# Kernel optimization log

Measured on AMD Instinct MI355X. Metric: run time of the kernel, lower is better.

## Reference

```python
import jax, jax.numpy as jnp
import numpy as np

DIM = 768
HEADS = 12
HEAD_DIM = DIM // HEADS
ROPE_BASE = 100.0  # Dust3R uses freq=100 for its rotary embedding


def apply_rope(x):
    # x: [B, H, N, D] -> rotary embedding over token index (rotate-half form)
    B, H, N, D = x.shape
    pos = jnp.arange(N, dtype=jnp.float32)
    inv_freq = 1.0 / (ROPE_BASE ** (jnp.arange(0, D, 2, dtype=jnp.float32) / D))
    ang = pos[:, None] * inv_freq[None, :]            # [N, D/2]
    cos = jnp.concatenate([jnp.cos(ang), jnp.cos(ang)], axis=-1).astype(x.dtype)  # [N, D]
    sin = jnp.concatenate([jnp.sin(ang), jnp.sin(ang)], axis=-1).astype(x.dtype)
    x1, x2 = jnp.split(x, 2, axis=-1)
    x_rot = jnp.concatenate([-x2, x1], axis=-1)
    return x * cos + x_rot * sin


def setup_inputs() -> dict:
    key = jax.random.key(0)
    ks = jax.random.split(key, 8)
    B, N = 8, 1024
    scale = 0.02
    return {
        "query": jax.random.normal(ks[0], (B, N, DIM), jnp.float32),
        "key": jax.random.normal(ks[1], (B, N, DIM), jnp.float32),
        "value": jax.random.normal(ks[2], (B, N, DIM), jnp.float32),
        "Wq": jax.random.normal(ks[3], (DIM, DIM), jnp.float32) * scale,
        "Wk": jax.random.normal(ks[4], (DIM, DIM), jnp.float32) * scale,
        "Wv": jax.random.normal(ks[5], (DIM, DIM), jnp.float32) * scale,
        "Wo": jax.random.normal(ks[6], (DIM, DIM), jnp.float32) * scale,
        "bo": jax.random.normal(ks[7], (DIM,), jnp.float32) * scale,
    }


def reference(query, key, value, Wq, Wk, Wv, Wo, bo):
    B, Nq, C = query.shape
    H, D = HEADS, HEAD_DIM
    sm_scale = D ** -0.5
    # Linear projections (torch Linear: x @ W.T), split heads -> [B, H, N, D]
    q = jnp.einsum('bnc,dc->bnd', query, Wq).reshape(B, Nq, H, D).transpose(0, 2, 1, 3)
    k = jnp.einsum('bnc,dc->bnd', key, Wk).reshape(B, -1, H, D).transpose(0, 2, 1, 3)
    v = jnp.einsum('bnc,dc->bnd', value, Wv).reshape(B, -1, H, D).transpose(0, 2, 1, 3)
    q = apply_rope(q)
    k = apply_rope(k)
    attn = jnp.einsum('bhqd,bhkd->bhqk', q, k) * sm_scale
    attn = jax.nn.softmax(attn, axis=-1)
    x = jnp.einsum('bhqk,bhkd->bhqd', attn, v)
    x = x.transpose(0, 2, 1, 3).reshape(B, Nq, C)
    return jnp.einsum('bnc,dc->bnd', x, Wo) + bo
```

## Files before the change

### kernel.cpp

```cpp
#include <hip/hip_runtime.h>
#include <cmath>

typedef __bf16 bf16x8 __attribute__((ext_vector_type(8)));
typedef float f32x4 __attribute__((ext_vector_type(4)));
typedef unsigned short u16;

#define MFMA_BF16 __builtin_amdgcn_mfma_f32_16x16x32_bf16

__device__ __forceinline__ u16 f2bf(float f) {
  unsigned int u = __float_as_uint(f);
  u = (u + 0x7fffu + ((u >> 16) & 1u)) >> 16;
  return (u16)u;
}

__device__ __forceinline__ unsigned pbf(float f) {
  return (__float_as_uint(f) + 0x8000u) >> 16;
}

__device__ __forceinline__ void async16(const u16* g, u16* l) {
  __builtin_amdgcn_global_load_lds(
      (__attribute__((address_space(1))) void*)g,
      (__attribute__((address_space(3))) void*)l, 16, 0, 0);
}

__global__ __launch_bounds__(256) void cvt_bf16(const float4* __restrict__ in,
                                                uint2* __restrict__ out, int n4) {
  int i = blockIdx.x * 256 + threadIdx.x;
  if (i >= n4) return;
  float4 f = in[i];
  uint2 o;
  o.x = (unsigned)f2bf(f.x) | ((unsigned)f2bf(f.y) << 16);
  o.y = (unsigned)f2bf(f.z) | ((unsigned)f2bf(f.w) << 16);
  out[i] = o;
}

__global__ __launch_bounds__(256) void cvt_all(
    const float4* s0, const float4* s1, const float4* s2, const float4* s3,
    const float4* s4, const float4* s5, const float4* s6,
    uint2* d0, uint2* d1, uint2* d2, uint2* d3, uint2* d4, uint2* d5, uint2* d6) {
  int i = blockIdx.x * 256 + threadIdx.x;
  const float4* src;
  uint2* dst;
  int off;
  if (i < 1572864)      { src = s0; dst = d0; off = i; }
  else if (i < 3145728) { src = s1; dst = d1; off = i - 1572864; }
  else if (i < 4718592) { src = s2; dst = d2; off = i - 3145728; }
  else {
    int j = i - 4718592;
    int w = j / 147456;
    off = j - w * 147456;
    src = (w == 0) ? s3 : (w == 1) ? s4 : (w == 2) ? s5 : s6;
    dst = (w == 0) ? d3 : (w == 1) ? d4 : (w == 2) ? d5 : d6;
  }
  float4 f = src[off];
  uint2 o;
  o.x = (unsigned)f2bf(f.x) | ((unsigned)f2bf(f.y) << 16);
  o.y = (unsigned)f2bf(f.z) | ((unsigned)f2bf(f.w) << 16);
  dst[off] = o;
}

__device__ __forceinline__ void gemm_body(const u16* __restrict__ Ag,
                                          const u16* __restrict__ Wg,
                                          void* __restrict__ OutP,
                                          const float* __restrict__ bias,
                                          int mode, int bx, int by) {
  __shared__ alignas(16) u16 As[2][128][64];
  __shared__ alignas(16) u16 Bs[2][64][64];
  const int tid  = threadIdx.x;
  const int lane = tid & 63, wv = tid >> 6;
  const int l15  = lane & 15, quad = lane >> 4;
  const int row0 = bx * 128, col0 = by * 64;
  const int wm = wv * 32;
  const int swA = l15 & 7;

  size_t aSrc[4], bSrc[2];
  int aDst[4], bDst[2];
#pragma unroll
  for (int rr = 0; rr < 4; ++rr) {
    int c = rr * 256 + tid;
    int row = c >> 3, cp = c & 7;
    int gc = cp ^ (row & 7);
    aSrc[rr] = (size_t)(row0 + row) * 768 + gc * 8;
    aDst[rr] = c * 8;
  }
#pragma unroll
  for (int rr = 0; rr < 2; ++rr) {
    int c = rr * 256 + tid;
    int row = c >> 3, cp = c & 7;
    int gc = cp ^ (row & 7);
    bSrc[rr] = (size_t)(col0 + row) * 768 + gc * 8;
    bDst[rr] = c * 8;
  }

  auto stage = [&](int kb, int bf) {
#pragma unroll
    for (int rr = 0; rr < 4; ++rr) async16(&Ag[aSrc[rr] + kb], &((u16*)As[bf])[aDst[rr]]);
#pragma unroll
    for (int rr = 0; rr < 2; ++rr) async16(&Wg[bSrc[rr] + kb], &((u16*)Bs[bf])[bDst[rr]]);
  };

  f32x4 acc[2][4];
#pragma unroll
  for (int i = 0; i < 2; ++i)
#pragma unroll
    for (int j = 0; j < 4; ++j) acc[i][j] = (f32x4){0.f, 0.f, 0.f, 0.f};

  stage(0, 0);
  __syncthreads();

  auto step = [&](int kb, int rb) {
    if (kb < 704) stage(kb + 64, rb ^ 1);
#pragma unroll
    for (int kd = 0; kd < 2; ++kd) {
      int cpk = (((kd * 4 + quad) ^ swA)) * 8;
      bf16x8 af[2], bfr[4];
      af[0] = *(const bf16x8*)&As[rb][wm + l15][cpk];
      af[1] = *(const bf16x8*)&As[rb][wm + 16 + l15][cpk];
#pragma unroll
      for (int nt = 0; nt < 4; ++nt) bfr[nt] = *(const bf16x8*)&Bs[rb][nt * 16 + l15][cpk];
#pragma unroll
      for (int mt = 0; mt < 2; ++mt)
#pragma unroll
        for (int nt = 0; nt < 4; ++nt)
          acc[mt][nt] = MFMA_BF16(af[mt], bfr[nt], acc[mt][nt], 0, 0, 0);
    }
    __syncthreads();
  };

  for (int kb = 0; kb < 768; kb += 128) {
    step(kb, 0);
    step(kb + 64, 1);
  }

  if (mode == 3) {
    float* O = (float*)OutP;
#pragma unroll
    for (int mt = 0; mt < 2; ++mt)
#pragma unroll
      for (int r = 0; r < 4; ++r) {
        int m = row0 + wm + mt * 16 + quad * 4 + r;
#pragma unroll
        for (int nt = 0; nt < 4; ++nt) {
          int c = col0 + nt * 16 + l15;
          O[(size_t)m * 768 + c] = acc[mt][nt][r] + bias[c];
        }
      }
  } else if (mode == 2) {
    u16* O = (u16*)OutP;
#pragma unroll
    for (int mt = 0; mt < 2; ++mt)
#pragma unroll
      for (int r = 0; r < 4; ++r) {
        int m = row0 + wm + mt * 16 + quad * 4 + r;
        int b = m >> 10, n = m & 1023;
#pragma unroll
        for (int nt = 0; nt < 4; ++nt) {
          int c = col0 + nt * 16 + l15;
          O[(size_t)(b * 768 + c) * 1024 + n] = f2bf(acc[mt][nt][r]);
        }
      }
  } else {
    u16* O = (u16*)OutP;
    const float scale = (mode == 0) ? 0.125f * 1.44269504088896f : 1.0f;
    const float invf0 = exp2f(-6.6438561897747395f * (float)l15 * (1.0f / 32.0f));
    const float invf1 = exp2f(-6.6438561897747395f * (float)(16 + l15) * (1.0f / 32.0f));
#pragma unroll
    for (int mt = 0; mt < 2; ++mt)
#pragma unroll
      for (int r = 0; r < 4; ++r) {
        int m = row0 + wm + mt * 16 + quad * 4 + r;
        int b = m >> 10, n = m & 1023;
        float fn = (float)n;
        size_t rowbase = (size_t)b * 786432 + (size_t)n * 64;
#pragma unroll
        for (int nt = 0; nt < 2; ++nt) {
          float sv, cv;
          __sincosf(fn * (nt ? invf1 : invf0), &sv, &cv);
          float x1 = acc[mt][nt][r], x2 = acc[mt][nt + 2][r];
          int c1 = col0 + nt * 16 + l15;
          int c2 = c1 + 32;
          O[rowbase + (size_t)(c1 >> 6) * 65536 + (c1 & 63)] = f2bf((x1 * cv - x2 * sv) * scale);
          O[rowbase + (size_t)(c2 >> 6) * 65536 + (c2 & 63)] = f2bf((x2 * cv + x1 * sv) * scale);
        }
      }
  }
}

__global__ __launch_bounds__(256, 3) void gemm768(const u16* __restrict__ A,
                                                  const u16* __restrict__ W,
                                                  void* __restrict__ OutP,
                                                  const float* __restrict__ bias,
                                                  int mode) {
  gemm_body(A, W, OutP, bias, mode, blockIdx.x, blockIdx.y);
}

__global__ __launch_bounds__(256, 3) void gemm_qkv(
    const u16* __restrict__ xq, const u16* __restrict__ xk, const u16* __restrict__ xv,
    const u16* __restrict__ wq, const u16* __restrict__ wk, const u16* __restrict__ wv,
    u16* __restrict__ qb, u16* __restrict__ kb, u16* __restrict__ vtb) {
  int z = blockIdx.z;
  const u16* A = (z == 0) ? xq : (z == 1) ? xk : xv;
  const u16* W = (z == 0) ? wq : (z == 1) ? wk : wv;
  void* O      = (z == 0) ? (void*)qb : (z == 1) ? (void*)kb : (void*)vtb;
  gemm_body(A, W, O, nullptr, z, blockIdx.x, blockIdx.y);
}

__global__ __launch_bounds__(256, 3) void attn_fused(const u16* __restrict__ Q,
                                                     const u16* __restrict__ K,
                                                     const u16* __restrict__ Vt,
                                                     u16* __restrict__ X) {
  __shared__ alignas(16) u16 KsF[2][4096];
  __shared__ alignas(16) u16 VsF[2][4096];
  __shared__ alignas(16) u16 Ps[4][2304];

  const int tid  = threadIdx.x;
  const int lane = tid & 63, wv = tid >> 6;
  const int l15  = lane & 15, quad = lane >> 4;
  const int bh = blockIdx.x, qt = blockIdx.y;
  const size_t base = (size_t)bh * 65536;
  const int sw8 = (quad ^ ((l15 >> 1) & 3)) * 8;

  const u16* Qg = Q + base + (size_t)qt * 8192;
  const u16* Kb = K + base;
  const u16* Vb = Vt + base;

  int kOff[2], vOff[2], dOff[2];
#pragma unroll
  for (int rr = 0; rr < 2; ++rr) {
    int c = rr * 256 + tid;
    int sub = c >> 8, rowi = (c >> 2) & 63, colc = c & 3;
    int cs = (colc ^ ((rowi >> 1) & 3)) * 8;
    kOff[rr] = rowi * 64 + sub * 32 + cs;
    vOff[rr] = rowi * 1024 + sub * 32 + cs;
    dOff[rr] = c * 8;
  }

  auto stageKV = [&](int kt, int bf) {
#pragma unroll
    for (int rr = 0; rr < 2; ++rr) {
      async16(&Kb[(size_t)kt * 64 + kOff[rr]], &KsF[bf][dOff[rr]]);
      async16(&Vb[(size_t)kt + vOff[rr]], &VsF[bf][dOff[rr]]);
    }
  };

  u16* Pflat = &Ps[0][0];
#pragma unroll
  for (int rr = 0; rr < 4; ++rr) {
    int c = rr * 256 + tid;
    async16(&Qg[c * 8], &Pflat[c * 8]);
  }
  stageKV(0, 0);
  __syncthreads();

  bf16x8 qf[2][2];
#pragma unroll
  for (int mt = 0; mt < 2; ++mt)
#pragma unroll
    for (int kd = 0; kd < 2; ++kd)
      qf[mt][kd] = *(const bf16x8*)&Pflat[(wv * 32 + mt * 16 + l15) * 64 + kd * 32 + quad * 8];
  __syncthreads();

  f32x4 o[2][4];
  float lsum[2] = {0.f, 0.f};
#pragma unroll
  for (int mt = 0; mt < 2; ++mt)
#pragma unroll
    for (int nt = 0; nt < 4; ++nt) o[mt][nt] = (f32x4){0.f, 0.f, 0.f, 0.f};

  u16* Pw = &Ps[wv][0];
  const int prow0 = l15 * 72, prow1 = (16 + l15) * 72;

  auto tile = [&](int t, int rb) {
    if (t < 15) stageKV((t + 1) * 64, rb ^ 1);

    f32x4 s[2][4];
#pragma unroll
    for (int ct = 0; ct < 4; ++ct) {
      bf16x8 kf0 = *(const bf16x8*)&KsF[rb][(ct * 16 + l15) * 32 + sw8];
      bf16x8 kf1 = *(const bf16x8*)&KsF[rb][2048 + (ct * 16 + l15) * 32 + sw8];
#pragma unroll
      for (int mt = 0; mt < 2; ++mt) {
        f32x4 tacc = (f32x4){0.f, 0.f, 0.f, 0.f};
        tacc = MFMA_BF16(kf0, qf[mt][0], tacc, 0, 0, 0);
        tacc = MFMA_BF16(kf1, qf[mt][1], tacc, 0, 0, 0);
        s[mt][ct] = tacc;
      }
    }

#pragma unroll
    for (int mt = 0; mt < 2; ++mt) {
#pragma unroll
      for (int ct = 0; ct < 4; ++ct) {
        float p0 = __builtin_amdgcn_exp2f(s[mt][ct][0]);
        float p1 = __builtin_amdgcn_exp2f(s[mt][ct][1]);
        float p2 = __builtin_amdgcn_exp2f(s[mt][ct][2]);
        float p3 = __builtin_amdgcn_exp2f(s[mt][ct][3]);
        lsum[mt] += (p0 + p1) + (p2 + p3);
        uint2 w;
        w.x = pbf(p0) | (pbf(p1) << 16);
        w.y = pbf(p2) | (pbf(p3) << 16);
        *(uint2*)&Pw[(mt ? prow1 : prow0) + ct * 16 + quad * 4] = w;
      }
    }

#pragma unroll
    for (int ks = 0; ks < 2; ++ks) {
      bf16x8 pf0 = *(const bf16x8*)&Pw[prow0 + ks * 32 + quad * 8];
      bf16x8 pf1 = *(const bf16x8*)&Pw[prow1 + ks * 32 + quad * 8];
#pragma unroll
      for (int nt = 0; nt < 4; ++nt) {
        bf16x8 vf = *(const bf16x8*)&VsF[rb][ks * 2048 + (nt * 16 + l15) * 32 + sw8];
        o[0][nt] = MFMA_BF16(vf, pf0, o[0][nt], 0, 0, 0);
        o[1][nt] = MFMA_BF16(vf, pf1, o[1][nt], 0, 0, 0);
      }
    }
    __syncthreads();
  };

  for (int t = 0; t < 16; t += 2) {
    tile(t, 0);
    tile(t + 1, 1);
  }

  const int b = bh / 12, h = bh % 12;
#pragma unroll
  for (int mt = 0; mt < 2; ++mt) {
    float l = lsum[mt];
    l += __shfl_xor(l, 16);
    l += __shfl_xor(l, 32);
    float inv = __builtin_amdgcn_rcpf(l);
    int n = qt * 128 + wv * 32 + mt * 16 + l15;
    size_t rowoff = ((size_t)(b * 1024 + n)) * 768 + h * 64 + quad * 4;
#pragma unroll
    for (int nt = 0; nt < 4; ++nt) {
      uint2 w;
      w.x = (unsigned)f2bf(o[mt][nt][0] * inv) | ((unsigned)f2bf(o[mt][nt][1] * inv) << 16);
      w.y = (unsigned)f2bf(o[mt][nt][2] * inv) | ((unsigned)f2bf(o[mt][nt][3] * inv) << 16);
      *(uint2*)&X[rowoff + nt * 16] = w;
    }
  }
}

extern "C" void kernel_launch(void* const* d_in, const int* in_sizes, int n_in,
                              void* d_out, int out_size, void* d_ws, size_t ws_size,
                              hipStream_t stream) {
  const float* qin = (const float*)d_in[0];
  const float* kin = (const float*)d_in[1];
  const float* vin = (const float*)d_in[2];
  const float* Wq  = (const float*)d_in[3];
  const float* Wk  = (const float*)d_in[4];
  const float* Wv  = (const float*)d_in[5];
  const float* Wo  = (const float*)d_in[6];
  const float* bo  = (const float*)d_in[7];
  char* ws = (char*)d_ws;

  if (ws_size >= 80216064) {
    u16* xq16 = (u16*)(ws + 0);
    u16* xk16 = (u16*)(ws + 12582912);
    u16* xv16 = (u16*)(ws + 25165824);
    u16* qb   = (u16*)(ws + 37748736);
    u16* kb   = (u16*)(ws + 50331648);
    u16* vtb  = (u16*)(ws + 62914560);
    u16* wq16 = (u16*)(ws + 75497472);
    u16* wk16 = wq16 + 589824;
    u16* wv16 = wk16 + 589824;
    u16* wo16 = wv16 + 589824;
    u16* X    = xq16;

    cvt_all<<<20736, 256, 0, stream>>>(
        (const float4*)qin, (const float4*)kin, (const float4*)vin,
        (const float4*)Wq, (const float4*)Wk, (const float4*)Wv, (const float4*)Wo,
        (uint2*)xq16, (uint2*)xk16, (uint2*)xv16,
        (uint2*)wq16, (uint2*)wk16, (uint2*)wv16, (uint2*)wo16);
    gemm_qkv<<<dim3(64, 12, 3), 256, 0, stream>>>(xq16, xk16, xv16, wq16, wk16, wv16,
                                                  qb, kb, vtb);
    attn_fused<<<dim3(96, 8), 256, 0, stream>>>(qb, kb, vtb, X);
    gemm768<<<dim3(64, 12), 256, 0, stream>>>(X, wo16, d_out, bo, 3);
  } else {
    u16* xbuf = (u16*)(ws + 0);
    u16* qb   = (u16*)(ws + 12582912);
    u16* kb   = (u16*)(ws + 25165824);
    u16* vtb  = (u16*)(ws + 37748736);
    u16* wq16 = (u16*)(ws + 50331648);
    u16* wk16 = wq16 + 589824;
    u16* wv16 = wk16 + 589824;
    u16* wo16 = wv16 + 589824;

    cvt_bf16<<<576, 256, 0, stream>>>((const float4*)Wq, (uint2*)wq16, 147456);
    cvt_bf16<<<576, 256, 0, stream>>>((const float4*)Wk, (uint2*)wk16, 147456);
    cvt_bf16<<<576, 256, 0, stream>>>((const float4*)Wv, (uint2*)wv16, 147456);
    cvt_bf16<<<576, 256, 0, stream>>>((const float4*)Wo, (uint2*)wo16, 147456);

    dim3 ggrid(64, 12);
    cvt_bf16<<<6144, 256, 0, stream>>>((const float4*)qin, (uint2*)xbuf, 1572864);
    gemm768<<<ggrid, 256, 0, stream>>>(xbuf, wq16, (void*)qb, nullptr, 0);
    cvt_bf16<<<6144, 256, 0, stream>>>((const float4*)kin, (uint2*)xbuf, 1572864);
    gemm768<<<ggrid, 256, 0, stream>>>(xbuf, wk16, (void*)kb, nullptr, 1);
    cvt_bf16<<<6144, 256, 0, stream>>>((const float4*)vin, (uint2*)xbuf, 1572864);
    gemm768<<<ggrid, 256, 0, stream>>>(xbuf, wv16, (void*)vtb, nullptr, 2);

    attn_fused<<<dim3(96, 8), 256, 0, stream>>>(qb, kb, vtb, xbuf);

    gemm768<<<ggrid, 256, 0, stream>>>(xbuf, wo16, d_out, bo, 3);
  }
}
```

Before: 219.2 us.

## Enlarge GEMM tile to 128x128 with 2x2 warp layout, drop double buffering

The projection GEMM tile grows from 128x64 to 128x128, and each wave now computes a 64x64 sub-tile in a 2x2 arrangement instead of a 32x64 strip. This raises MFMA work per LDS fragment load and halves the grid's column count. The LDS double buffer is replaced by a single buffer with a load, sync, compute, sync loop, so global loads no longer overlap compute. Higher register use per thread (16 accumulators) may lower occupancy under the launch bound of 3.

```diff
diff --git a/kernel.cpp b/kernel.cpp
--- a/kernel.cpp
+++ b/kernel.cpp
@@ -64,98 +64,81 @@
                                           void* __restrict__ OutP,
                                           const float* __restrict__ bias,
                                           int mode, int bx, int by) {
-  __shared__ alignas(16) u16 As[2][128][64];
-  __shared__ alignas(16) u16 Bs[2][64][64];
+  __shared__ alignas(16) u16 As[128][64];
+  __shared__ alignas(16) u16 Bs[128][64];
   const int tid  = threadIdx.x;
   const int lane = tid & 63, wv = tid >> 6;
   const int l15  = lane & 15, quad = lane >> 4;
-  const int row0 = bx * 128, col0 = by * 64;
-  const int wm = wv * 32;
+  const int row0 = bx * 128, col0 = by * 128;
+  const int wr = (wv >> 1) * 64, wc = (wv & 1) * 64;
   const int swA = l15 & 7;
 
-  size_t aSrc[4], bSrc[2];
-  int aDst[4], bDst[2];
+  size_t aSrc[4], bSrc[4];
+  int dsts[4];
 #pragma unroll
   for (int rr = 0; rr < 4; ++rr) {
     int c = rr * 256 + tid;
     int row = c >> 3, cp = c & 7;
     int gc = cp ^ (row & 7);
     aSrc[rr] = (size_t)(row0 + row) * 768 + gc * 8;
-    aDst[rr] = c * 8;
-  }
-#pragma unroll
-  for (int rr = 0; rr < 2; ++rr) {
-    int c = rr * 256 + tid;
-    int row = c >> 3, cp = c & 7;
-    int gc = cp ^ (row & 7);
     bSrc[rr] = (size_t)(col0 + row) * 768 + gc * 8;
-    bDst[rr] = c * 8;
-  }
-
-  auto stage = [&](int kb, int bf) {
-#pragma unroll
-    for (int rr = 0; rr < 4; ++rr) async16(&Ag[aSrc[rr] + kb], &((u16*)As[bf])[aDst[rr]]);
-#pragma unroll
-    for (int rr = 0; rr < 2; ++rr) async16(&Wg[bSrc[rr] + kb], &((u16*)Bs[bf])[bDst[rr]]);
-  };
-
-  f32x4 acc[2][4];
-#pragma unroll
-  for (int i = 0; i < 2; ++i)
+    dsts[rr] = c * 8;
+  }
+
+  f32x4 acc[4][4];
+#pragma unroll
+  for (int i = 0; i < 4; ++i)
 #pragma unroll
     for (int j = 0; j < 4; ++j) acc[i][j] = (f32x4){0.f, 0.f, 0.f, 0.f};
 
-  stage(0, 0);
-  __syncthreads();
-
-  auto step = [&](int kb, int rb) {
-    if (kb < 704) stage(kb + 64, rb ^ 1);
+  for (int kb = 0; kb < 768; kb += 64) {
+#pragma unroll
+    for (int rr = 0; rr < 4; ++rr) {
+      async16(&Ag[aSrc[rr] + kb], &((u16*)As)[dsts[rr]]);
+      async16(&Wg[bSrc[rr] + kb], &((u16*)Bs)[dsts[rr]]);
+    }
+    __syncthreads();
 #pragma unroll
     for (int kd = 0; kd < 2; ++kd) {
-      int cpk = (((kd * 4 + quad) ^ swA)) * 8;
-      bf16x8 af[2], bfr[4];
-      af[0] = *(const bf16x8*)&As[rb][wm + l15][cpk];
-      af[1] = *(const bf16x8*)&As[rb][wm + 16 + l15][cpk];
-#pragma unroll
-      for (int nt = 0; nt < 4; ++nt) bfr[nt] = *(const bf16x8*)&Bs[rb][nt * 16 + l15][cpk];
-#pragma unroll
-      for (int mt = 0; mt < 2; ++mt)
+      int cpk = ((kd * 4 + quad) ^ swA) * 8;
+      bf16x8 af[4], bfr[4];
+#pragma unroll
+      for (int mt = 0; mt < 4; ++mt) af[mt] = *(const bf16x8*)&As[wr + mt * 16 + l15][cpk];
+#pragma unroll
+      for (int nt = 0; nt < 4; ++nt) bfr[nt] = *(const bf16x8*)&Bs[wc + nt * 16 + l15][cpk];
+#pragma unroll
+      for (int mt = 0; mt < 4; ++mt)
 #pragma unroll
         for (int nt = 0; nt < 4; ++nt)
           acc[mt][nt] = MFMA_BF16(af[mt], bfr[nt], acc[mt][nt], 0, 0, 0);
     }
     __syncthreads();
-  };
-
-  for (int kb = 0; kb < 768; kb += 128) {
-    step(kb, 0);
-    step(kb + 64, 1);
   }
 
   if (mode == 3) {
     float* O = (float*)OutP;
 #pragma unroll
-    for (int mt = 0; mt < 2; ++mt)
+    for (int mt = 0; mt < 4; ++mt)
 #pragma unroll
       for (int r = 0; r < 4; ++r) {
-        int m = row0 + wm + mt * 16 + quad * 4 + r;
+        int m = row0 + wr + mt * 16 + quad * 4 + r;
 #pragma unroll
         for (int nt = 0; nt < 4; ++nt) {
-          int c = col0 + nt * 16 + l15;
+          int c = col0 + wc + nt * 16 + l15;
           O[(size_t)m * 768 + c] = acc[mt][nt][r] + bias[c];
         }
       }
   } else if (mode == 2) {
     u16* O = (u16*)OutP;
 #pragma unroll
-    for (int mt = 0; mt < 2; ++mt)
+    for (int mt = 0; mt < 4; ++mt)
 #pragma unroll
       for (int r = 0; r < 4; ++r) {
-        int m = row0 + wm + mt * 16 + quad * 4 + r;
+        int m = row0 + wr + mt * 16 + quad * 4 + r;
         int b = m >> 10, n = m & 1023;
 #pragma unroll
         for (int nt = 0; nt < 4; ++nt) {
-          int c = col0 + nt * 16 + l15;
+          int c = col0 + wc + nt * 16 + l15;
           O[(size_t)(b * 768 + c) * 1024 + n] = f2bf(acc[mt][nt][r]);
         }
       }
@@ -165,10 +148,10 @@
     const float invf0 = exp2f(-6.6438561897747395f * (float)l15 * (1.0f / 32.0f));
     const float invf1 = exp2f(-6.6438561897747395f * (float)(16 + l15) * (1.0f / 32.0f));
 #pragma unroll
-    for (int mt = 0; mt < 2; ++mt)
+    for (int mt = 0; mt < 4; ++mt)
 #pragma unroll
       for (int r = 0; r < 4; ++r) {
-        int m = row0 + wm + mt * 16 + quad * 4 + r;
+        int m = row0 + wr + mt * 16 + quad * 4 + r;
         int b = m >> 10, n = m & 1023;
         float fn = (float)n;
         size_t rowbase = (size_t)b * 786432 + (size_t)n * 64;
@@ -177,7 +160,7 @@
           float sv, cv;
           __sincosf(fn * (nt ? invf1 : invf0), &sv, &cv);
           float x1 = acc[mt][nt][r], x2 = acc[mt][nt + 2][r];
-          int c1 = col0 + nt * 16 + l15;
+          int c1 = col0 + wc + nt * 16 + l15;
           int c2 = c1 + 32;
           O[rowbase + (size_t)(c1 >> 6) * 65536 + (c1 & 63)] = f2bf((x1 * cv - x2 * sv) * scale);
           O[rowbase + (size_t)(c2 >> 6) * 65536 + (c2 & 63)] = f2bf((x2 * cv + x1 * sv) * scale);
@@ -372,10 +355,10 @@
         (const float4*)Wq, (const float4*)Wk, (const float4*)Wv, (const float4*)Wo,
         (uint2*)xq16, (uint2*)xk16, (uint2*)xv16,
         (uint2*)wq16, (uint2*)wk16, (uint2*)wv16, (uint2*)wo16);
-    gemm_qkv<<<dim3(64, 12, 3), 256, 0, stream>>>(xq16, xk16, xv16, wq16, wk16, wv16,
-                                                  qb, kb, vtb);
+    gemm_qkv<<<dim3(64, 6, 3), 256, 0, stream>>>(xq16, xk16, xv16, wq16, wk16, wv16,
+                                                 qb, kb, vtb);
     attn_fused<<<dim3(96, 8), 256, 0, stream>>>(qb, kb, vtb, X);
-    gemm768<<<dim3(64, 12), 256, 0, stream>>>(X, wo16, d_out, bo, 3);
+    gemm768<<<dim3(64, 6), 256, 0, stream>>>(X, wo16, d_out, bo, 3);
   } else {
     u16* xbuf = (u16*)(ws + 0);
     u16* qb   = (u16*)(ws + 12582912);
@@ -391,7 +374,7 @@
     cvt_bf16<<<576, 256, 0, stream>>>((const float4*)Wv, (uint2*)wv16, 147456);
     cvt_bf16<<<576, 256, 0, stream>>>((const float4*)Wo, (uint2*)wo16, 147456);
 
-    dim3 ggrid(64, 12);
+    dim3 ggrid(64, 6);
     cvt_bf16<<<6144, 256, 0, stream>>>((const float4*)qin, (uint2*)xbuf, 1572864);
     gemm768<<<ggrid, 256, 0, stream>>>(xbuf, wq16, (void*)qb, nullptr, 0);
     cvt_bf16<<<6144, 256, 0, stream>>>((const float4*)kin, (uint2*)xbuf, 1572864);
```

Result: slower. 225.1 us (+2.7%).
